# Performance work log

Hardware: AMD Instinct MI355X
Metric: run time of the kernel (lower is better)

Reference implementation:

```python
import jax, jax.numpy as jnp
import numpy as np

B, S, E, H, DH = 4, 2048, 2048, 16, 256  # DH = mlp hidden (d_hid)
HD = E // H  # per-head dim = 128
EPS = 1e-5

def _ln(x, w, b):
    m = jnp.mean(x, axis=-1, keepdims=True)
    v = jnp.mean(jnp.square(x - m), axis=-1, keepdims=True)
    return (x - m) * jax.lax.rsqrt(v + EPS) * w + b

def setup_inputs() -> dict:
    key = jax.random.key(0)
    ks = jax.random.split(key, 10)
    s = 0.02
    return {
        "x": jax.random.normal(ks[0], (B, S, E), jnp.float32),
        "attention_mask": jax.random.randint(ks[1], (B, S), 0, 2, jnp.int32),
        "ln1_w": jnp.ones((E,), jnp.float32),
        "ln1_b": jnp.zeros((E,), jnp.float32),
        "in_proj_w": jax.random.normal(ks[2], (3 * E, E), jnp.float32) * s,
        "in_proj_b": jnp.zeros((3 * E,), jnp.float32),
        "out_proj_w": jax.random.normal(ks[3], (E, E), jnp.float32) * s,
        "out_proj_b": jnp.zeros((E,), jnp.float32),
        "ln2_w": jnp.ones((E,), jnp.float32),
        "ln2_b": jnp.zeros((E,), jnp.float32),
        "mlp_w1": jax.random.normal(ks[4], (DH, E), jnp.float32) * s,
        "mlp_b1": jnp.zeros((DH,), jnp.float32),
        "mlp_w2": jax.random.normal(ks[5], (E, DH), jnp.float32) * s,
        "mlp_b2": jnp.zeros((E,), jnp.float32),
    }

def reference(x, attention_mask, ln1_w, ln1_b, in_proj_w, in_proj_b,
              out_proj_w, out_proj_b, ln2_w, ln2_b, mlp_w1, mlp_b1, mlp_w2, mlp_b2):
    h = _ln(x, ln1_w, ln1_b)
    qkv = h @ in_proj_w.T + in_proj_b  # [B,S,3E]
    q, k, v = jnp.split(qkv, 3, axis=-1)
    q = q.reshape(B, S, H, HD).transpose(0, 2, 1, 3) / jnp.sqrt(jnp.float32(HD))
    k = k.reshape(B, S, H, HD).transpose(0, 2, 1, 3)
    v = v.reshape(B, S, H, HD).transpose(0, 2, 1, 3)
    scores = jnp.einsum("bhqd,bhkd->bhqk", q, k)
    # Faithful to source: FLOAT attn_mask of +1.0 on strictly-upper triangle (additive),
    # NOT -inf; key_padding_mask positions do get -inf.
    causal_add = jnp.triu(jnp.ones((S, S), jnp.float32), k=1)
    scores = scores + causal_add
    pad = (attention_mask == 0)  # True = padded key
    scores = jnp.where(pad[:, None, None, :], jnp.float32(-jnp.inf), scores)
    attn = jax.nn.softmax(scores, axis=-1)
    ctx = jnp.einsum("bhqk,bhkd->bhqd", attn, v)
    ctx = ctx.transpose(0, 2, 1, 3).reshape(B, S, E)
    x = x + ctx @ out_proj_w.T + out_proj_b
    h2 = _ln(x, ln2_w, ln2_b)
    mlp = jax.nn.relu(h2 @ mlp_w1.T + mlp_b1) @ mlp_w2.T + mlp_b2
    return x + mlp
```

## Files before the change

kernel.cpp:

```cpp
#include <hip/hip_runtime.h>

typedef __attribute__((ext_vector_type(8))) short short8;
typedef __attribute__((ext_vector_type(4))) float f32x4;
typedef __attribute__((ext_vector_type(16))) float f32x16;

typedef __attribute__((address_space(1))) const void gas1_t;
typedef __attribute__((address_space(3))) void las3_t;
#define GLL16(g, l) __builtin_amdgcn_global_load_lds((gas1_t*)(g), (las3_t*)(l), 16, 0, 0)

__device__ inline unsigned short f2bf(float f) {
  union { float f; unsigned int u; } v; v.f = f;
  unsigned int r = v.u + 0x7FFFu + ((v.u >> 16) & 1u);
  return (unsigned short)(r >> 16);
}

__device__ inline float exp2_fast(float x) {
  float r; asm("v_exp_f32 %0, %1" : "=v"(r) : "v"(x)); return r;
}

__device__ inline void vmwait(int n) {
  if (n == 6)      asm volatile("s_waitcnt vmcnt(6)" ::: "memory");
  else if (n == 4) asm volatile("s_waitcnt vmcnt(4)" ::: "memory");
  else             asm volatile("s_waitcnt vmcnt(0)" ::: "memory");
}

__global__ __launch_bounds__(256) void ln_kernel(const float* __restrict__ x,
                                                 const float* __restrict__ w,
                                                 const float* __restrict__ bia,
                                                 unsigned short* __restrict__ out) {
  const int row = blockIdx.x;
  const int tid = threadIdx.x;
  const float* xr = x + (size_t)row * 2048;
  float4 a = *(const float4*)(xr + tid * 8);
  float4 b = *(const float4*)(xr + tid * 8 + 4);
  float s  = a.x + a.y + a.z + a.w + b.x + b.y + b.z + b.w;
  float s2 = a.x*a.x + a.y*a.y + a.z*a.z + a.w*a.w + b.x*b.x + b.y*b.y + b.z*b.z + b.w*b.w;
  #pragma unroll
  for (int off = 1; off < 64; off <<= 1) {
    s  += __shfl_xor(s, off);
    s2 += __shfl_xor(s2, off);
  }
  __shared__ float red[8];
  if ((tid & 63) == 0) { red[tid >> 6] = s; red[4 + (tid >> 6)] = s2; }
  __syncthreads();
  s  = red[0] + red[1] + red[2] + red[3];
  s2 = red[4] + red[5] + red[6] + red[7];
  const float mean = s * (1.f / 2048.f);
  const float var  = s2 * (1.f / 2048.f) - mean * mean;
  const float rstd = rsqrtf(var + 1e-5f);
  float4 wa = *(const float4*)(w + tid * 8), wb = *(const float4*)(w + tid * 8 + 4);
  float4 ba = *(const float4*)(bia + tid * 8), bb = *(const float4*)(bia + tid * 8 + 4);
  short8 o;
  o[0] = (short)f2bf((a.x - mean) * rstd * wa.x + ba.x);
  o[1] = (short)f2bf((a.y - mean) * rstd * wa.y + ba.y);
  o[2] = (short)f2bf((a.z - mean) * rstd * wa.z + ba.z);
  o[3] = (short)f2bf((a.w - mean) * rstd * wa.w + ba.w);
  o[4] = (short)f2bf((b.x - mean) * rstd * wb.x + bb.x);
  o[5] = (short)f2bf((b.y - mean) * rstd * wb.y + bb.y);
  o[6] = (short)f2bf((b.z - mean) * rstd * wb.z + bb.z);
  o[7] = (short)f2bf((b.w - mean) * rstd * wb.w + bb.w);
  *(short8*)(out + (size_t)row * 2048 + tid * 8) = o;
}

__global__ __launch_bounds__(256) void conv_kernel(const float* __restrict__ in,
                                                   unsigned short* __restrict__ out, int n) {
  size_t idx = ((size_t)blockIdx.x * 256 + threadIdx.x) * 8;
  if (idx >= (size_t)n) return;
  float4 a = *(const float4*)(in + idx);
  float4 b = *(const float4*)(in + idx + 4);
  short8 o;
  o[0] = (short)f2bf(a.x); o[1] = (short)f2bf(a.y);
  o[2] = (short)f2bf(a.z); o[3] = (short)f2bf(a.w);
  o[4] = (short)f2bf(b.x); o[5] = (short)f2bf(b.y);
  o[6] = (short)f2bf(b.z); o[7] = (short)f2bf(b.w);
  *(short8*)(out + idx) = o;
}

template <int MODE>
__global__ __launch_bounds__(256) void gemm_bt(const unsigned short* __restrict__ A,
                                               const unsigned short* __restrict__ Bw,
                                               const float* __restrict__ bias,
                                               const float* __restrict__ res,
                                               void* __restrict__ outp,
                                               void* __restrict__ outp2,
                                               int M, int N, int K) {
  __shared__ unsigned short As[128 * 64];
  __shared__ unsigned short Bs[128 * 64];
  const int tid = threadIdx.x;
  const int l = tid & 63, wv = tid >> 6;
  const int l15 = l & 15, l4 = l >> 4;
  const int wr = wv >> 1, wc = wv & 1;
  const int nx = gridDim.x;
  const int nwg = nx * gridDim.y;
  const int bidlin = blockIdx.y * nx + blockIdx.x;
  const int cpx = nwg >> 3;
  const int swz = (bidlin & 7) * cpx + (bidlin >> 3);
  const int m0 = (swz / nx) * 128, n0 = (swz % nx) * 128;

  f32x4 acc[4][4] = {};
  for (int k0 = 0; k0 < K; k0 += 64) {
    __syncthreads();
    #pragma unroll
    for (int i = 0; i < 4; ++i) {
      int e = i * 2048 + tid * 8;
      int r = e >> 6;
      int c = (e ^ ((r & 7) << 3)) & 63;
      GLL16(A + (size_t)(m0 + r) * K + k0 + c, As + e);
      GLL16(Bw + (size_t)(n0 + r) * K + k0 + c, Bs + e);
    }
    __syncthreads();
    #pragma unroll
    for (int kk = 0; kk < 64; kk += 32) {
      short8 af[4], bfr[4];
      #pragma unroll
      for (int m = 0; m < 4; ++m) {
        int r = wr * 64 + m * 16 + l15;
        int byt = (r * 128 + (kk + l4 * 8) * 2) ^ ((r & 7) << 4);
        af[m] = *(const short8*)((const char*)As + byt);
      }
      #pragma unroll
      for (int n = 0; n < 4; ++n) {
        int r = wc * 64 + n * 16 + l15;
        int byt = (r * 128 + (kk + l4 * 8) * 2) ^ ((r & 7) << 4);
        bfr[n] = *(const short8*)((const char*)Bs + byt);
      }
      #pragma unroll
      for (int m = 0; m < 4; ++m)
        #pragma unroll
        for (int n = 0; n < 4; ++n)
          acc[m][n] = __builtin_amdgcn_mfma_f32_16x16x32_bf16(af[m], bfr[n], acc[m][n], 0, 0, 0);
    }
  }
  #pragma unroll
  for (int m = 0; m < 4; ++m) {
    #pragma unroll
    for (int n = 0; n < 4; ++n) {
      #pragma unroll
      for (int r = 0; r < 4; ++r) {
        int row = m0 + wr * 64 + m * 16 + l4 * 4 + r;
        int col = n0 + wc * 64 + n * 16 + l15;
        float v = acc[m][n][r] + bias[col];
        if (MODE == 1) {
          ((unsigned short*)outp)[(size_t)row * N + col] = f2bf(v > 0.f ? v : 0.f);
        } else {
          ((float*)outp)[(size_t)row * N + col] = res[(size_t)row * N + col] + v;
        }
      }
    }
  }
}

template <int MODE>
__global__ __launch_bounds__(512, 2) void gemm8(const unsigned short* __restrict__ A,
                                                const unsigned short* __restrict__ Bw,
                                                const float* __restrict__ bias,
                                                const float* __restrict__ res,
                                                void* __restrict__ outp,
                                                void* __restrict__ outp2,
                                                int M, int N, int K) {
  __shared__ char LA[2][2][16384];
  __shared__ char LB[2][2][16384];
  const int tid = threadIdx.x;
  const int l = tid & 63, wv = tid >> 6;
  const int l15 = l & 15, l4 = l >> 4;
  const int wr = wv >> 2, wc = wv & 3;
  const int nx = gridDim.x;
  const int nwg = nx * gridDim.y;
  const int bidlin = blockIdx.y * nx + blockIdx.x;
  const int cpx = nwg >> 3;
  const int swz = (bidlin & 7) * cpx + (bidlin >> 3);
  const int m0 = (swz / nx) * 256, n0 = (swz % nx) * 256;

  int srow0, scol0, srow1, scol1;
  {
    int o = tid * 16, p = o >> 7, i = o & 127;
    srow0 = 2 * p + ((i >> 6) & 1);
    scol0 = (((i >> 4) & 3) ^ (p & 3)) * 8;
    o = 8192 + tid * 16; p = o >> 7; i = o & 127;
    srow1 = 2 * p + ((i >> 6) & 1);
    scol1 = (((i >> 4) & 3) ^ (p & 3)) * 8;
  }

#define STG_A(t, kh) { int kk = (t) * 64 + (kh) * 32; \
    GLL16(A + (size_t)(m0 + srow0) * K + kk + scol0, &LA[(t) & 1][kh][tid * 16]); \
    GLL16(A + (size_t)(m0 + srow1) * K + kk + scol1, &LA[(t) & 1][kh][8192 + tid * 16]); }
#define STG_B(t, kh) { int kk = (t) * 64 + (kh) * 32; \
    GLL16(Bw + (size_t)(n0 + srow0) * K + kk + scol0, &LB[(t) & 1][kh][tid * 16]); \
    GLL16(Bw + (size_t)(n0 + srow1) * K + kk + scol1, &LB[(t) & 1][kh][8192 + tid * 16]); }

#define LDSOFF(r, c4) (((r) >> 1) * 128 + (((((r) & 1) << 6) + ((c4) << 4)) ^ ((((r) >> 1) & 3) << 4)))

  f32x4 acc[8][4] = {};
  const int NT = K >> 6, iters = NT >> 1;

  STG_A(0, 0); STG_B(0, 0); STG_A(0, 1); STG_B(0, 1); STG_A(1, 0);
  vmwait(6);
  __builtin_amdgcn_s_barrier();

#define PH(t, kh, mh, STG, VM) { \
    short8 af[4], bf[4]; \
    const char* Ab = LA[(t) & 1][kh]; \
    const char* Bb = LB[(t) & 1][kh]; \
    _Pragma("unroll") for (int f = 0; f < 4; ++f) { \
      int ra = wr * 128 + ((mh) * 4 + f) * 16 + l15; \
      af[f] = *(const short8*)(Ab + LDSOFF(ra, l4)); \
      int rb = wc * 64 + f * 16 + l15; \
      bf[f] = *(const short8*)(Bb + LDSOFF(rb, l4)); } \
    STG; \
    __builtin_amdgcn_s_barrier(); \
    asm volatile("s_waitcnt lgkmcnt(0)" ::: "memory"); \
    __builtin_amdgcn_sched_barrier(0); \
    __builtin_amdgcn_s_setprio(1); \
    _Pragma("unroll") for (int f = 0; f < 4; ++f) \
      _Pragma("unroll") for (int n = 0; n < 4; ++n) \
        acc[(mh) * 4 + f][n] = __builtin_amdgcn_mfma_f32_16x16x32_bf16(af[f], bf[n], acc[(mh) * 4 + f][n], 0, 0, 0); \
    __builtin_amdgcn_s_setprio(0); \
    if ((VM) >= 0) vmwait(VM); \
    __builtin_amdgcn_s_barrier(); }

  for (int i = 0; i < iters; ++i) {
    const int T0 = 2 * i, T1 = 2 * i + 1, T2 = 2 * i + 2, T3 = 2 * i + 3;
    const bool last = (i == iters - 1);
    PH(T0, 0, 0, STG_B(T1, 0), -1);
    PH(T0, 0, 1, STG_A(T1, 1), 6);
    PH(T0, 1, 0, STG_B(T1, 1), -1);
    PH(T0, 1, 1, if (T2 < NT) STG_A(T2, 0), last ? 4 : 6);
    PH(T1, 0, 0, if (T2 < NT) STG_B(T2, 0), -1);
    PH(T1, 0, 1, if (T2 < NT) STG_A(T2, 1), last ? 0 : 6);
    PH(T1, 1, 0, if (T2 < NT) STG_B(T2, 1), -1);
    PH(T1, 1, 1, if (T3 < NT) STG_A(T3, 0), last ? -1 : 6);
  }
#undef PH
#undef STG_A
#undef STG_B
#undef LDSOFF

  #pragma unroll
  for (int mf = 0; mf < 8; ++mf) {
    #pragma unroll
    for (int nf = 0; nf < 4; ++nf) {
      #pragma unroll
      for (int r = 0; r < 4; ++r) {
        int row = m0 + wr * 128 + mf * 16 + l4 * 4 + r;
        int col = n0 + wc * 64 + nf * 16 + l15;
        float v = acc[mf][nf][r] + bias[col];
        if (MODE == 0) {
          unsigned short val = f2bf(v);
          if (col < 4096) ((unsigned short*)outp)[(size_t)row * 4096 + col] = val;
          else            ((unsigned short*)outp2)[(size_t)row * 2048 + col - 4096] = val;
        } else {
          ((float*)outp)[(size_t)row * N + col] = res[(size_t)row * N + col] + v;
        }
      }
    }
  }
}

__global__ __launch_bounds__(256) void vtrans_kernel(const unsigned short* __restrict__ v,
                                                     unsigned short* __restrict__ vT) {
  __shared__ unsigned short T[128 * 128];
  const int t0 = blockIdx.x * 128;
  const int b = blockIdx.y >> 4, h = blockIdx.y & 15;
  const int tid = threadIdx.x;
  const int tl = tid >> 4, l16 = tid & 15, c8 = l16 * 8;
  #pragma unroll
  for (int i = 0; i < 8; ++i) {
    int t = tl + i * 16;
    short8 val = *(const short8*)(v + (size_t)(b * 2048 + t0 + t) * 2048 + h * 128 + c8);
    *(short8*)((char*)T + ((t * 256 + c8 * 2) ^ ((t & 7) << 4))) = val;
  }
  __syncthreads();
  #pragma unroll
  for (int i = 0; i < 8; ++i) {
    int d = tl + i * 16;
    unsigned short* orow = vT + ((size_t)(b * 16 + h) * 128 + d) * 2048 + t0;
    #pragma unroll
    for (int j = 0; j < 8; ++j) {
      int t = l16 + 16 * j;
      orow[t] = *(const unsigned short*)((const char*)T + ((t * 256 + d * 2) ^ ((t & 7) << 4)));
    }
  }
}

__global__ __launch_bounds__(256) void attn_kernel(const unsigned short* __restrict__ qk,
                                                   const unsigned short* __restrict__ vT,
                                                   const int* __restrict__ amask,
                                                   unsigned short* __restrict__ ctx) {
  __shared__ unsigned short Ks[2][4096];
  __shared__ unsigned short Vs[2][4096];
  __shared__ unsigned short Pl[4][1152];

  const int qt = blockIdx.x, bh = blockIdx.y;
  const int b = bh >> 4, h = bh & 15;
  const int tid = threadIdx.x;
  const int wv = tid >> 6, l = tid & 63;
  const int l31 = l & 31, hi = l >> 5;
  const int q0w = qt * 128 + wv * 32;
  const float SC2 = 0.08838834764831845f * 1.4426950408889634f;
  const float L2E = 1.4426950408889634f;
  const float MF  = 10.0f;

  int kinv[2], vinv[2];
  #pragma unroll
  for (int c = 0; c < 2; ++c) {
    int e = c * 2048 + tid * 8;
    int key = e >> 7, d0 = e & 127;
    kinv[c] = key * 4096 + 2048 + h * 128 + (d0 ^ ((key & 7) << 3));
    int d = e >> 5, kchunk = ((e >> 3) & 3) ^ ((d & 6) >> 1);
    vinv[c] = d * 2048 + kchunk * 8;
  }
  const unsigned short* kb0 = qk + (size_t)(b * 2048) * 4096;
  const unsigned short* vb0 = vT + (size_t)(b * 16 + h) * (128 * 2048);
  const int* mrow = amask + b * 2048;

  short8 qf[8];
  {
    const unsigned short* qp = qk + (size_t)(b * 2048 + q0w + l31) * 4096 + h * 128 + hi * 8;
    #pragma unroll
    for (int c = 0; c < 8; ++c) qf[c] = *(const short8*)(qp + c * 16);
  }

  short8 vones;
  #pragma unroll
  for (int j = 0; j < 8; ++j) vones[j] = (short)0x3F80;

  f32x16 o[4] = {};
  f32x16 ol = {};

  #pragma unroll
  for (int c = 0; c < 2; ++c) {
    GLL16(kb0 + kinv[c], &Ks[0][c * 2048 + tid * 8]);
    GLL16(vb0 + vinv[c], &Vs[0][c * 2048 + tid * 8]);
  }
  __syncthreads();

  for (int kt = 0; kt < 2048; kt += 32) {
    const int cur = (kt >> 5) & 1;
    if (kt + 32 < 2048) {
      #pragma unroll
      for (int c = 0; c < 2; ++c) {
        GLL16(kb0 + (size_t)(kt + 32) * 4096 + kinv[c], &Ks[cur ^ 1][c * 2048 + tid * 8]);
        GLL16(vb0 + (kt + 32) + vinv[c], &Vs[cur ^ 1][c * 2048 + tid * 8]);
      }
    }
    const bool pad = (mrow[kt + l31] == 0);

    f32x16 sacc = {};
    __builtin_amdgcn_s_setprio(1);
    #pragma unroll
    for (int c = 0; c < 8; ++c) {
      short8 kf = *(const short8*)((const char*)Ks[cur] +
                   ((l31 * 256 + c * 32 + hi * 16) ^ ((l31 & 7) << 4)));
      sacc = __builtin_amdgcn_mfma_f32_32x32x16_bf16(qf[c], kf, sacc, 0, 0, 0);
    }
    __builtin_amdgcn_s_setprio(0);

    float s[16];
    if (kt > q0w + 31) {
      #pragma unroll
      for (int i = 0; i < 16; ++i) s[i] = sacc[i] * SC2 + L2E;
    } else if (kt + 31 <= q0w) {
      #pragma unroll
      for (int i = 0; i < 16; ++i) s[i] = sacc[i] * SC2;
    } else {
      int kg = kt + l31;
      #pragma unroll
      for (int i = 0; i < 16; ++i) {
        int qg = q0w + (i & 3) + 8 * (i >> 2) + 4 * hi;
        s[i] = sacc[i] * SC2 + ((kg > qg) ? L2E : 0.f);
      }
    }
    if (pad) {
      #pragma unroll
      for (int i = 0; i < 16; ++i) s[i] = -1e30f;
    }

    #pragma unroll
    for (int i = 0; i < 16; ++i) {
      int q = (i & 3) + 8 * (i >> 2) + 4 * hi;
      Pl[wv][q * 36 + l31] = f2bf(exp2_fast(s[i] - MF));
    }
    short8 pa0 = *(const short8*)&Pl[wv][l31 * 36 + hi * 8];
    short8 pa1 = *(const short8*)&Pl[wv][l31 * 36 + 16 + hi * 8];

    __builtin_amdgcn_s_setprio(1);
    #pragma unroll
    for (int g = 0; g < 4; ++g) {
      int d = g * 32 + l31;
      int swzd = (d & 6) << 3;
      short8 vf0 = *(const short8*)((const char*)Vs[cur] + ((d * 64 + hi * 16) ^ swzd));
      o[g] = __builtin_amdgcn_mfma_f32_32x32x16_bf16(pa0, vf0, o[g], 0, 0, 0);
      short8 vf1 = *(const short8*)((const char*)Vs[cur] + ((d * 64 + 32 + hi * 16) ^ swzd));
      o[g] = __builtin_amdgcn_mfma_f32_32x32x16_bf16(pa1, vf1, o[g], 0, 0, 0);
    }
    ol = __builtin_amdgcn_mfma_f32_32x32x16_bf16(pa0, vones, ol, 0, 0, 0);
    ol = __builtin_amdgcn_mfma_f32_32x32x16_bf16(pa1, vones, ol, 0, 0, 0);
    __builtin_amdgcn_s_setprio(0);

    __syncthreads();
  }

  float inv[16];
  #pragma unroll
  for (int i = 0; i < 16; ++i) inv[i] = 1.0f / ol[i];
  #pragma unroll
  for (int g = 0; g < 4; ++g) {
    #pragma unroll
    for (int i = 0; i < 16; ++i) {
      int q = q0w + (i & 3) + 8 * (i >> 2) + 4 * hi;
      ctx[(size_t)(b * 2048 + q) * 2048 + h * 128 + g * 32 + l31] = f2bf(o[g][i] * inv[i]);
    }
  }
}

extern "C" void kernel_launch(void* const* d_in, const int* in_sizes, int n_in,
                              void* d_out, int out_size, void* d_ws, size_t ws_size,
                              hipStream_t stream) {
  (void)in_sizes; (void)n_in; (void)out_size; (void)ws_size;
  const float* x    = (const float*)d_in[0];
  const int*   am   = (const int*)d_in[1];
  const float* ln1w = (const float*)d_in[2];
  const float* ln1b = (const float*)d_in[3];
  const float* win  = (const float*)d_in[4];
  const float* bin  = (const float*)d_in[5];
  const float* wout = (const float*)d_in[6];
  const float* bout = (const float*)d_in[7];
  const float* ln2w = (const float*)d_in[8];
  const float* ln2b = (const float*)d_in[9];
  const float* w1   = (const float*)d_in[10];
  const float* b1   = (const float*)d_in[11];
  const float* w2   = (const float*)d_in[12];
  const float* b2   = (const float*)d_in[13];
  float* out = (float*)d_out;

  char* ws = (char*)d_ws;
  unsigned short* hbuf = (unsigned short*)ws;
  unsigned short* vTb  = (unsigned short*)ws;
  unsigned short* qkb  = (unsigned short*)(ws + (size_t)32 * 1048576);
  unsigned short* h2b  = (unsigned short*)(ws + (size_t)32 * 1048576);
  unsigned short* midb = (unsigned short*)(ws + (size_t)64 * 1048576);
  unsigned short* vbuf = (unsigned short*)(ws + (size_t)96 * 1048576);
  unsigned short* ctxb = (unsigned short*)(ws + (size_t)96 * 1048576);
  unsigned short* wbuf = (unsigned short*)(ws + (size_t)128 * 1048576);

  ln_kernel<<<dim3(8192), dim3(256), 0, stream>>>(x, ln1w, ln1b, hbuf);
  conv_kernel<<<dim3(6144), dim3(256), 0, stream>>>(win, wbuf, 12582912);
  gemm8<0><<<dim3(24, 32), dim3(512), 0, stream>>>(hbuf, wbuf, bin, (const float*)nullptr,
                                                   (void*)qkb, (void*)vbuf, 8192, 6144, 2048);
  vtrans_kernel<<<dim3(16, 64), dim3(256), 0, stream>>>(vbuf, vTb);
  attn_kernel<<<dim3(16, 64), dim3(256), 0, stream>>>(qkb, vTb, am, ctxb);
  conv_kernel<<<dim3(2048), dim3(256), 0, stream>>>(wout, wbuf, 4194304);
  gemm8<2><<<dim3(8, 32), dim3(512), 0, stream>>>(ctxb, wbuf, bout, x,
                                                  (void*)out, nullptr, 8192, 2048, 2048);
  ln_kernel<<<dim3(8192), dim3(256), 0, stream>>>(out, ln2w, ln2b, h2b);
  conv_kernel<<<dim3(256), dim3(256), 0, stream>>>(w1, wbuf, 524288);
  gemm_bt<1><<<dim3(2, 64), dim3(256), 0, stream>>>(h2b, wbuf, b1, (const float*)nullptr,
                                                    (void*)midb, nullptr, 8192, 256, 2048);
  conv_kernel<<<dim3(256), dim3(256), 0, stream>>>(w2, wbuf, 524288);
  gemm_bt<2><<<dim3(16, 64), dim3(256), 0, stream>>>(midb, wbuf, b2, out,
                                                     (void*)out, nullptr, 8192, 2048, 256);
}
```

Baseline: 655.2 us.

## Restructure GEMM mainloop to full-K64 tile per stage with register fragment reuse

Rewrites the gemm8 main loop so that each LDS buffer holds a 128-row by 64-k half-tile with a new 8-way XOR swizzle. Each wave loads its A and B fragments for both k-halves once and reuses them across four MFMA quarter-blocks, instead of reloading fragments in eight phases per pair of k-tiles. Global-to-LDS staging is re-sequenced between the MFMA quarters with new barrier placement and vmcnt waits. The aim is fewer LDS reads and barriers per MFMA. In exchange, register pressure rises, and the tighter staging and wait ordering could expose more load latency.

```diff
diff --git a/kernel.cpp b/kernel.cpp
--- a/kernel.cpp
+++ b/kernel.cpp
@@ -20,7 +20,6 @@
 
 __device__ inline void vmwait(int n) {
   if (n == 6)      asm volatile("s_waitcnt vmcnt(6)" ::: "memory");
-  else if (n == 4) asm volatile("s_waitcnt vmcnt(4)" ::: "memory");
   else             asm volatile("s_waitcnt vmcnt(0)" ::: "memory");
 }
 
@@ -164,6 +163,7 @@
   const int l = tid & 63, wv = tid >> 6;
   const int l15 = l & 15, l4 = l >> 4;
   const int wr = wv >> 2, wc = wv & 3;
+  const int wch = wc >> 1, wcl = wc & 1;
   const int nx = gridDim.x;
   const int nwg = nx * gridDim.y;
   const int bidlin = blockIdx.y * nx + blockIdx.x;
@@ -171,69 +171,77 @@
   const int swz = (bidlin & 7) * cpx + (bidlin >> 3);
   const int m0 = (swz / nx) * 256, n0 = (swz % nx) * 256;
 
-  int srow0, scol0, srow1, scol1;
-  {
-    int o = tid * 16, p = o >> 7, i = o & 127;
-    srow0 = 2 * p + ((i >> 6) & 1);
-    scol0 = (((i >> 4) & 3) ^ (p & 3)) * 8;
-    o = 8192 + tid * 16; p = o >> 7; i = o & 127;
-    srow1 = 2 * p + ((i >> 6) & 1);
-    scol1 = (((i >> 4) & 3) ^ (p & 3)) * 8;
-  }
-
-#define STG_A(t, kh) { int kk = (t) * 64 + (kh) * 32; \
-    GLL16(A + (size_t)(m0 + srow0) * K + kk + scol0, &LA[(t) & 1][kh][tid * 16]); \
-    GLL16(A + (size_t)(m0 + srow1) * K + kk + scol1, &LA[(t) & 1][kh][8192 + tid * 16]); }
-#define STG_B(t, kh) { int kk = (t) * 64 + (kh) * 32; \
-    GLL16(Bw + (size_t)(n0 + srow0) * K + kk + scol0, &LB[(t) & 1][kh][tid * 16]); \
-    GLL16(Bw + (size_t)(n0 + srow1) * K + kk + scol1, &LB[(t) & 1][kh][8192 + tid * 16]); }
-
-#define LDSOFF(r, c4) (((r) >> 1) * 128 + (((((r) & 1) << 6) + ((c4) << 4)) ^ ((((r) >> 1) & 3) << 4)))
+  const int srow = tid >> 3;
+  const int scol = ((tid & 7) ^ (srow & 7)) * 8;
+
+#define STG_A(x, h) { const unsigned short* bp = A + (size_t)(m0 + (h) * 128) * K + (x) * 64; \
+    GLL16(bp + (size_t)srow * K + scol, &LA[(x) & 1][h][tid * 16]); \
+    GLL16(bp + (size_t)(srow + 64) * K + scol, &LA[(x) & 1][h][8192 + tid * 16]); }
+#define STG_B(x, h) { const unsigned short* bp = Bw + (size_t)(n0 + (h) * 128) * K + (x) * 64; \
+    GLL16(bp + (size_t)srow * K + scol, &LB[(x) & 1][h][tid * 16]); \
+    GLL16(bp + (size_t)(srow + 64) * K + scol, &LB[(x) & 1][h][8192 + tid * 16]); }
+
+#define FOFF(r, kh) ((r) * 128 + (((((kh) * 4 + l4)) ^ ((r) & 7)) << 4))
 
   f32x4 acc[8][4] = {};
-  const int NT = K >> 6, iters = NT >> 1;
-
-  STG_A(0, 0); STG_B(0, 0); STG_A(0, 1); STG_B(0, 1); STG_A(1, 0);
+  const int NT = K >> 6;
+
+  STG_A(0, 0); STG_A(0, 1); STG_B(0, 0); STG_B(0, 1);
+  STG_B(1, 0); STG_B(1, 1); STG_A(1, 0);
   vmwait(6);
   __builtin_amdgcn_s_barrier();
 
-#define PH(t, kh, mh, STG, VM) { \
-    short8 af[4], bf[4]; \
-    const char* Ab = LA[(t) & 1][kh]; \
-    const char* Bb = LB[(t) & 1][kh]; \
-    _Pragma("unroll") for (int f = 0; f < 4; ++f) { \
-      int ra = wr * 128 + ((mh) * 4 + f) * 16 + l15; \
-      af[f] = *(const short8*)(Ab + LDSOFF(ra, l4)); \
-      int rb = wc * 64 + f * 16 + l15; \
-      bf[f] = *(const short8*)(Bb + LDSOFF(rb, l4)); } \
-    STG; \
-    __builtin_amdgcn_s_barrier(); \
-    asm volatile("s_waitcnt lgkmcnt(0)" ::: "memory"); \
-    __builtin_amdgcn_sched_barrier(0); \
+#define MFMAQ(mh, nh) \
     __builtin_amdgcn_s_setprio(1); \
-    _Pragma("unroll") for (int f = 0; f < 4; ++f) \
-      _Pragma("unroll") for (int n = 0; n < 4; ++n) \
-        acc[(mh) * 4 + f][n] = __builtin_amdgcn_mfma_f32_16x16x32_bf16(af[f], bf[n], acc[(mh) * 4 + f][n], 0, 0, 0); \
-    __builtin_amdgcn_s_setprio(0); \
-    if ((VM) >= 0) vmwait(VM); \
-    __builtin_amdgcn_s_barrier(); }
-
-  for (int i = 0; i < iters; ++i) {
-    const int T0 = 2 * i, T1 = 2 * i + 1, T2 = 2 * i + 2, T3 = 2 * i + 3;
-    const bool last = (i == iters - 1);
-    PH(T0, 0, 0, STG_B(T1, 0), -1);
-    PH(T0, 0, 1, STG_A(T1, 1), 6);
-    PH(T0, 1, 0, STG_B(T1, 1), -1);
-    PH(T0, 1, 1, if (T2 < NT) STG_A(T2, 0), last ? 4 : 6);
-    PH(T1, 0, 0, if (T2 < NT) STG_B(T2, 0), -1);
-    PH(T1, 0, 1, if (T2 < NT) STG_A(T2, 1), last ? 0 : 6);
-    PH(T1, 1, 0, if (T2 < NT) STG_B(T2, 1), -1);
-    PH(T1, 1, 1, if (T3 < NT) STG_A(T3, 0), last ? -1 : 6);
-  }
-#undef PH
+    _Pragma("unroll") for (int kh = 0; kh < 2; ++kh) \
+      _Pragma("unroll") for (int f = 0; f < 4; ++f) \
+        _Pragma("unroll") for (int n = 0; n < 2; ++n) \
+          acc[(mh) * 4 + f][(nh) * 2 + n] = __builtin_amdgcn_mfma_f32_16x16x32_bf16( \
+              af[kh][f], bfr[kh][(nh) * 2 + n], acc[(mh) * 4 + f][(nh) * 2 + n], 0, 0, 0); \
+    __builtin_amdgcn_s_setprio(0);
+
+  for (int t = 0; t < NT; ++t) {
+    const char* Ab = LA[t & 1][wr];
+    const char* Bb = LB[t & 1][wch];
+    short8 af[2][4], bfr[2][4];
+    #pragma unroll
+    for (int kh = 0; kh < 2; ++kh)
+      #pragma unroll
+      for (int f = 0; f < 4; ++f) {
+        af[kh][f] = *(const short8*)(Ab + FOFF(f * 16 + l15, kh));
+        bfr[kh][f] = *(const short8*)(Bb + FOFF(wcl * 64 + f * 16 + l15, kh));
+      }
+    if (t + 1 < NT) STG_A(t + 1, 1);
+    __builtin_amdgcn_s_barrier();
+    asm volatile("s_waitcnt lgkmcnt(0)" ::: "memory");
+    __builtin_amdgcn_sched_barrier(0);
+    MFMAQ(0, 0);
+    __builtin_amdgcn_s_barrier();
+    if (t + 2 < NT) STG_B(t + 2, 0);
+    __builtin_amdgcn_s_barrier();
+    MFMAQ(0, 1);
+    __builtin_amdgcn_s_barrier();
+    #pragma unroll
+    for (int kh = 0; kh < 2; ++kh)
+      #pragma unroll
+      for (int f = 0; f < 4; ++f)
+        af[kh][f] = *(const short8*)(Ab + FOFF(64 + f * 16 + l15, kh));
+    if (t + 2 < NT) STG_B(t + 2, 1);
+    __builtin_amdgcn_s_barrier();
+    asm volatile("s_waitcnt lgkmcnt(0)" ::: "memory");
+    __builtin_amdgcn_sched_barrier(0);
+    MFMAQ(1, 0);
+    __builtin_amdgcn_s_barrier();
+    if (t + 2 < NT) STG_A(t + 2, 0);
+    __builtin_amdgcn_s_barrier();
+    MFMAQ(1, 1);
+    vmwait(t >= NT - 2 ? 0 : 6);
+    __builtin_amdgcn_s_barrier();
+  }
+#undef MFMAQ
+#undef FOFF
 #undef STG_A
 #undef STG_B
-#undef LDSOFF
 
   #pragma unroll
   for (int mf = 0; mf < 8; ++mf) {
```

Result: faster. 631.2 us (-3.7%).
